# Optimization experiments

Measured on AMD Instinct MI355X. Metric: run time of the kernel, lower is better.

## Reference

```python
import jax, jax.numpy as jnp
import numpy as np

HIDDEN = 4096
NUM_HEADS = 32
NUM_KV_HEADS = 8
HEAD_DIM = 128
ROTARY_DIM = HEAD_DIM // 2  # partial_rotary_factor = 0.5
ROPE_THETA = 10000.0
EPS = 1e-5
T = 2048
Q_SIZE = NUM_HEADS * HEAD_DIM      # 4096
KV_SIZE = NUM_KV_HEADS * HEAD_DIM  # 1024


def setup_inputs() -> dict:
    key = jax.random.key(0)
    ks = jax.random.split(key, 6)
    s_in = 1.0 / np.sqrt(HIDDEN)
    s_o = 1.0 / np.sqrt(Q_SIZE)
    return {
        "positions": jnp.arange(T, dtype=jnp.int64),
        "hidden_states": jax.random.normal(ks[0], (T, HIDDEN), dtype=jnp.float32),
        "w_qkv": jax.random.normal(ks[1], (Q_SIZE + 2 * KV_SIZE, HIDDEN), dtype=jnp.float32) * s_in,
        "b_qkv": jax.random.normal(ks[2], (Q_SIZE + 2 * KV_SIZE,), dtype=jnp.float32) * 0.02,
        "q_norm_w": jnp.ones((HEAD_DIM,), dtype=jnp.float32),
        "k_norm_w": jnp.ones((HEAD_DIM,), dtype=jnp.float32),
        "w_o": jax.random.normal(ks[3], (HIDDEN, Q_SIZE), dtype=jnp.float32) * s_o,
    }


def _rms_norm(x, w, eps=EPS):
    # x: [..., head_dim]
    var = jnp.mean(x * x, axis=-1, keepdims=True)
    return x * jax.lax.rsqrt(var + eps) * w


def _apply_rope(x, positions):
    # x: [T, H, head_dim]; NeoX-style rotation on first ROTARY_DIM dims
    half = ROTARY_DIM // 2
    inv_freq = 1.0 / (ROPE_THETA ** (jnp.arange(0, ROTARY_DIM, 2, dtype=jnp.float32) / ROTARY_DIM))
    freqs = positions.astype(jnp.float32)[:, None] * inv_freq[None, :]  # [T, half]
    cos = jnp.cos(freqs)[:, None, :]  # [T, 1, half]
    sin = jnp.sin(freqs)[:, None, :]
    x_rot, x_pass = x[..., :ROTARY_DIM], x[..., ROTARY_DIM:]
    x1, x2 = x_rot[..., :half], x_rot[..., half:]
    rot = jnp.concatenate([x1 * cos - x2 * sin, x2 * cos + x1 * sin], axis=-1)
    return jnp.concatenate([rot, x_pass], axis=-1)


def reference(positions, hidden_states, w_qkv, b_qkv, q_norm_w, k_norm_w, w_o):
    qkv = hidden_states @ w_qkv.T + b_qkv  # [T, Q+2KV]
    q = qkv[:, :Q_SIZE].reshape(T, NUM_HEADS, HEAD_DIM)
    k = qkv[:, Q_SIZE:Q_SIZE + KV_SIZE].reshape(T, NUM_KV_HEADS, HEAD_DIM)
    v = qkv[:, Q_SIZE + KV_SIZE:].reshape(T, NUM_KV_HEADS, HEAD_DIM)

    q = _rms_norm(q, q_norm_w)
    k = _rms_norm(k, k_norm_w)

    q = _apply_rope(q, positions)
    k = _apply_rope(k, positions)

    # GQA: expand kv heads to match q heads
    rep = NUM_HEADS // NUM_KV_HEADS
    k = jnp.repeat(k, rep, axis=1)  # [T, H, D]
    v = jnp.repeat(v, rep, axis=1)

    scale = HEAD_DIM ** -0.5
    scores = jnp.einsum('qhd,khd->hqk', q, k) * scale  # [H, T, T]
    causal = positions[:, None] >= positions[None, :]  # [T, T]
    scores = jnp.where(causal[None, :, :], scores, jnp.float32(-1e30))
    probs = jax.nn.softmax(scores, axis=-1)
    attn = jnp.einsum('hqk,khd->qhd', probs, v).reshape(T, Q_SIZE)
    return attn @ w_o.T
```

## Files before the change

kernel.cpp:

```cpp
#include <hip/hip_runtime.h>
#include <stdint.h>

#define T_SEQ 2048
#define HIDDEN 4096
#define NUM_HEADS 32
#define NUM_KV 8
#define HD 128
#define QSIZE (NUM_HEADS * HD)
#define KVSIZE (NUM_KV * HD)
#define QKV_N (QSIZE + 2 * KVSIZE)

typedef __attribute__((ext_vector_type(8))) __bf16 bf16x8;
typedef __attribute__((ext_vector_type(4))) float f32x4;

static __device__ __forceinline__ unsigned short f2bf(float f) {
  union { float f; unsigned int u; } v; v.f = f;
  unsigned int u = v.u;
  return (unsigned short)((u + 0x7FFFu + ((u >> 16) & 1u)) >> 16);
}

static __device__ __forceinline__ void async16(const void* g, void* l) {
  __builtin_amdgcn_global_load_lds((__attribute__((address_space(1))) void*)g,
                                   (__attribute__((address_space(3))) void*)l,
                                   16, 0, 0);
}

static __device__ __forceinline__ bf16x8 lds_frag(const unsigned short* p) {
  return *(const bf16x8*)p;
}

#define N1 (T_SEQ * HIDDEN / 4)
#define N2 (QKV_N * HIDDEN / 4)
#define N3 (HIDDEN * QSIZE / 4)
__global__ void cvt_all(const float* __restrict__ h,
                        const float* __restrict__ wq,
                        const float* __restrict__ wo,
                        unsigned short* __restrict__ hb,
                        unsigned short* __restrict__ wqb,
                        unsigned short* __restrict__ wob) {
  int i = blockIdx.x * 256 + threadIdx.x;
  const float* src;
  unsigned short* dst;
  int j;
  if (i < N1) { src = h; dst = hb; j = i; }
  else if (i < N1 + N2) { src = wq; dst = wqb; j = i - N1; }
  else { src = wo; dst = wob; j = i - N1 - N2; }
  float4 f = ((const float4*)src)[j];
  ushort4 o;
  o.x = f2bf(f.x); o.y = f2bf(f.y); o.z = f2bf(f.z); o.w = f2bf(f.w);
  ((ushort4*)dst)[j] = o;
}

__global__ __launch_bounds__(256) void gemm_bt(
    const unsigned short* __restrict__ A,
    const unsigned short* __restrict__ Bt,
    const float* __restrict__ bias,
    float* __restrict__ C, int M, int N, int K) {
  __shared__ unsigned short lds_a[128 * 32];
  __shared__ unsigned short lds_b[128 * 32];
  const int tid = threadIdx.x;
  const int wave = tid >> 6, lane = tid & 63;
  const int quad = lane >> 4, l16 = lane & 15;
  const int row0 = blockIdx.x * 128, col0 = blockIdx.y * 128;
  const int wm = (wave >> 1) * 64, wn = (wave & 1) * 64;

  f32x4 acc[4][4] = {};

  const int e0 = wave * 1024 + lane * 8;
  const int e1 = e0 + 512;
  const unsigned short* Ab0 = A + (size_t)(row0 + (e0 >> 5)) * K + (e0 & 31);
  const unsigned short* Ab1 = A + (size_t)(row0 + (e1 >> 5)) * K + (e1 & 31);
  const unsigned short* Bb0 = Bt + (size_t)(col0 + (e0 >> 5)) * K + (e0 & 31);
  const unsigned short* Bb1 = Bt + (size_t)(col0 + (e1 >> 5)) * K + (e1 & 31);
  unsigned short* la0 = lds_a + wave * 1024;
  unsigned short* la1 = la0 + 512;
  unsigned short* lb0 = lds_b + wave * 1024;
  unsigned short* lb1 = lb0 + 512;

  for (int k0 = 0; k0 < K; k0 += 32) {
    __syncthreads();
    async16(Ab0 + k0, la0);
    async16(Ab1 + k0, la1);
    async16(Bb0 + k0, lb0);
    async16(Bb1 + k0, lb1);
    __syncthreads();
    bf16x8 af[4], bfr[4];
#pragma unroll
    for (int mt = 0; mt < 4; mt++)
      af[mt] = lds_frag(lds_a + (wm + mt * 16 + l16) * 32 + quad * 8);
#pragma unroll
    for (int nt = 0; nt < 4; nt++)
      bfr[nt] = lds_frag(lds_b + (wn + nt * 16 + l16) * 32 + quad * 8);
#pragma unroll
    for (int mt = 0; mt < 4; mt++)
#pragma unroll
      for (int nt = 0; nt < 4; nt++)
        acc[mt][nt] = __builtin_amdgcn_mfma_f32_16x16x32_bf16(
            af[mt], bfr[nt], acc[mt][nt], 0, 0, 0);
  }

#pragma unroll
  for (int mt = 0; mt < 4; mt++) {
#pragma unroll
    for (int nt = 0; nt < 4; nt++) {
      const int c = col0 + wn + nt * 16 + l16;
      const float bv = bias ? bias[c] : 0.0f;
      const int rbase = row0 + wm + mt * 16 + quad * 4;
#pragma unroll
      for (int r = 0; r < 4; r++)
        C[(size_t)(rbase + r) * N + c] = acc[mt][nt][r] + bv;
    }
  }
}

__global__ __launch_bounds__(256) void gemm_bt_splitk(
    const unsigned short* __restrict__ A,
    const unsigned short* __restrict__ Bt,
    float* __restrict__ C, int M, int N, int K, int kslice) {
  __shared__ unsigned short lds_a[128 * 32];
  __shared__ unsigned short lds_b[128 * 32];
  const int tid = threadIdx.x;
  const int wave = tid >> 6, lane = tid & 63;
  const int quad = lane >> 4, l16 = lane & 15;
  const int row0 = blockIdx.x * 128, col0 = blockIdx.y * 128;
  const int kofs = blockIdx.z * kslice;
  const int wm = (wave >> 1) * 64, wn = (wave & 1) * 64;

  f32x4 acc[4][4] = {};

  const int e0 = wave * 1024 + lane * 8;
  const int e1 = e0 + 512;
  const unsigned short* Ab0 = A + (size_t)(row0 + (e0 >> 5)) * K + kofs + (e0 & 31);
  const unsigned short* Ab1 = A + (size_t)(row0 + (e1 >> 5)) * K + kofs + (e1 & 31);
  const unsigned short* Bb0 = Bt + (size_t)(col0 + (e0 >> 5)) * K + kofs + (e0 & 31);
  const unsigned short* Bb1 = Bt + (size_t)(col0 + (e1 >> 5)) * K + kofs + (e1 & 31);
  unsigned short* la0 = lds_a + wave * 1024;
  unsigned short* la1 = la0 + 512;
  unsigned short* lb0 = lds_b + wave * 1024;
  unsigned short* lb1 = lb0 + 512;

  for (int k0 = 0; k0 < kslice; k0 += 32) {
    __syncthreads();
    async16(Ab0 + k0, la0);
    async16(Ab1 + k0, la1);
    async16(Bb0 + k0, lb0);
    async16(Bb1 + k0, lb1);
    __syncthreads();
    bf16x8 af[4], bfr[4];
#pragma unroll
    for (int mt = 0; mt < 4; mt++)
      af[mt] = lds_frag(lds_a + (wm + mt * 16 + l16) * 32 + quad * 8);
#pragma unroll
    for (int nt = 0; nt < 4; nt++)
      bfr[nt] = lds_frag(lds_b + (wn + nt * 16 + l16) * 32 + quad * 8);
#pragma unroll
    for (int mt = 0; mt < 4; mt++)
#pragma unroll
      for (int nt = 0; nt < 4; nt++)
        acc[mt][nt] = __builtin_amdgcn_mfma_f32_16x16x32_bf16(
            af[mt], bfr[nt], acc[mt][nt], 0, 0, 0);
  }

#pragma unroll
  for (int mt = 0; mt < 4; mt++) {
#pragma unroll
    for (int nt = 0; nt < 4; nt++) {
      const int c = col0 + wn + nt * 16 + l16;
      const int rbase = row0 + wm + mt * 16 + quad * 4;
#pragma unroll
      for (int r = 0; r < 4; r++)
        unsafeAtomicAdd(&C[(size_t)(rbase + r) * N + c], acc[mt][nt][r]);
    }
  }
}

__global__ void norm_rope(const float* __restrict__ qkv,
                          const float* __restrict__ qw,
                          const float* __restrict__ kw,
                          unsigned short* __restrict__ q,
                          unsigned short* __restrict__ k) {
  const int slot = blockIdx.x;
  const int t = blockIdx.y;
  const int d = threadIdx.x;
  const float* src = (slot < 32)
      ? qkv + (size_t)t * QKV_N + slot * HD
      : qkv + (size_t)t * QKV_N + QSIZE + (slot - 32) * HD;
  float x = src[d];
  __shared__ float red[2];
  __shared__ float ylds[HD];
  float ss = x * x;
#pragma unroll
  for (int m = 32; m >= 1; m >>= 1) ss += __shfl_xor(ss, m, 64);
  if ((d & 63) == 0) red[d >> 6] = ss;
  __syncthreads();
  const float rn = rsqrtf((red[0] + red[1]) * (1.0f / 128.0f) + 1e-5f);
  const float* w = (slot < 32) ? qw : kw;
  const float y = x * rn * w[d];
  ylds[d] = y;
  __syncthreads();
  float out;
  if (d < 64) {
    const int j = d & 31;
    const float inv = exp2f(-(float)j * (13.28771237954945f / 32.0f));
    const float ang = (float)t * inv;
    float s, c;
    sincosf(ang, &s, &c);
    const float x1 = ylds[j], x2 = ylds[j + 32];
    out = (d < 32) ? (x1 * c - x2 * s) : (x2 * c + x1 * s);
  } else {
    out = y;
  }
  if (slot < 32) q[((size_t)slot * T_SEQ + t) * HD + d] = f2bf(out);
  else           k[((size_t)(slot - 32) * T_SEQ + t) * HD + d] = f2bf(out);
}

__global__ __launch_bounds__(256) void transpose_v(
    const float* __restrict__ qkv, unsigned short* __restrict__ vt) {
  __shared__ unsigned short tile[64 * 136];
  const int kvh = blockIdx.x, tt = blockIdx.y;
  const int tid = threadIdx.x;
  {
    const int t_r = tid >> 2, d0 = (tid & 3) * 32;
    const float* src = qkv + (size_t)(tt * 64 + t_r) * QKV_N +
                       (QSIZE + KVSIZE) + kvh * HD + d0;
#pragma unroll
    for (int i = 0; i < 8; i++) {
      float4 f = ((const float4*)src)[i];
      unsigned short* dptr = tile + t_r * 136 + d0 + i * 4;
      dptr[0] = f2bf(f.x); dptr[1] = f2bf(f.y);
      dptr[2] = f2bf(f.z); dptr[3] = f2bf(f.w);
    }
  }
  __syncthreads();
  {
    const int d_r = tid >> 1, t0 = (tid & 1) * 32;
    unsigned short buf[32];
#pragma unroll
    for (int i = 0; i < 32; i++) buf[i] = tile[(t0 + i) * 136 + d_r];
    uint4* dst = (uint4*)(vt + ((size_t)kvh * HD + d_r) * T_SEQ + tt * 64 + t0);
#pragma unroll
    for (int i = 0; i < 4; i++) dst[i] = ((uint4*)buf)[i];
  }
}

#define BC 64
#define KCH 528
#define VCH 544
#define PST 72
__global__ __launch_bounds__(256) void attn_fwd(
    const unsigned short* __restrict__ Q,
    const unsigned short* __restrict__ K,
    const unsigned short* __restrict__ Vt,
    unsigned short* __restrict__ O) {
  __shared__ unsigned short lds_k[16 * KCH];
  __shared__ unsigned short lds_v[16 * VCH];
  __shared__ unsigned short lds_p[4 * 32 * PST];

  const int bx = blockIdx.x;
  const int qb = 15 - (bx >> 5);
  const int h = bx & 31;
  const int kvh = h >> 2;
  const int tid = threadIdx.x, wave = tid >> 6, lane = tid & 63;
  const int quad = lane >> 4, l16 = lane & 15;
  const int q0 = qb * 128;
  const int mrow0 = q0 + wave * 32;

  bf16x8 qf[2][4];
#pragma unroll
  for (int m = 0; m < 2; m++) {
    const unsigned short* qp =
        Q + ((size_t)h * T_SEQ + mrow0 + m * 16 + l16) * HD + quad * 8;
#pragma unroll
    for (int c2 = 0; c2 < 4; c2++) qf[m][c2] = *(const bf16x8*)(qp + c2 * 32);
  }

  f32x4 o_acc[2][8] = {};
  float lrow[2][4] = {};
  const float l2e_s = 1.4426950408889634f * 0.08838834764831845f;
  const float FMAX = 129.0f;
  const unsigned short* kb = K + (size_t)kvh * T_SEQ * HD;
  const unsigned short* vtb = Vt + (size_t)kvh * HD * T_SEQ;
  unsigned short* pbase = lds_p + wave * 32 * PST;

  const int nkt = 2 * (qb + 1);
  for (int kt = 0; kt < nkt; kt++) {
    const int kbase = kt * BC;
    __syncthreads();
#pragma unroll
    for (int cc = 0; cc < 4; cc++) {
      const int c = wave + cc * 4;
      async16(kb + (size_t)(kbase + c * 4 + (lane >> 4)) * HD + (lane & 15) * 8,
              lds_k + c * KCH + lane * 8);
      async16(vtb + (size_t)(c * 8 + (lane >> 3)) * T_SEQ + kbase + (lane & 7) * 8,
              lds_v + c * VCH + lane * 8);
    }
    __syncthreads();

    if (kbase > mrow0 + 31) continue;

    f32x4 s[2][4] = {};
#pragma unroll
    for (int c2 = 0; c2 < 4; c2++) {
#pragma unroll
      for (int nt = 0; nt < 4; nt++) {
        bf16x8 kf = lds_frag(lds_k + (nt * 4 + (l16 >> 2)) * KCH +
                             (l16 & 3) * 128 + c2 * 32 + quad * 8);
        s[0][nt] = __builtin_amdgcn_mfma_f32_16x16x32_bf16(qf[0][c2], kf, s[0][nt], 0, 0, 0);
        s[1][nt] = __builtin_amdgcn_mfma_f32_16x16x32_bf16(qf[1][c2], kf, s[1][nt], 0, 0, 0);
      }
    }

    const bool domask = (kbase + 63 > mrow0);
#pragma unroll
    for (int m = 0; m < 2; m++) {
#pragma unroll
      for (int r = 0; r < 4; r++) {
        const int row = mrow0 + m * 16 + quad * 4 + r;
        float ps = 0.f;
        unsigned short* pw = pbase + (m * 16 + quad * 4 + r) * PST + l16;
#pragma unroll
        for (int nt = 0; nt < 4; nt++) {
          float x = s[m][nt][r];
          if (domask && (kbase + nt * 16 + l16 > row)) x = -INFINITY;
          const float p = exp2f((x - FMAX) * l2e_s);
          ps += p;
          pw[nt * 16] = f2bf(p);
        }
        lrow[m][r] += ps;
      }
    }

#pragma unroll
    for (int ks = 0; ks < 2; ks++) {
      bf16x8 pa0 = lds_frag(pbase + l16 * PST + ks * 32 + quad * 8);
      bf16x8 pa1 = lds_frag(pbase + (16 + l16) * PST + ks * 32 + quad * 8);
#pragma unroll
      for (int dt = 0; dt < 8; dt++) {
        bf16x8 vf = lds_frag(lds_v + (dt * 2 + (l16 >> 3)) * VCH +
                             (l16 & 7) * 64 + ks * 32 + quad * 8);
        o_acc[0][dt] = __builtin_amdgcn_mfma_f32_16x16x32_bf16(pa0, vf, o_acc[0][dt], 0, 0, 0);
        o_acc[1][dt] = __builtin_amdgcn_mfma_f32_16x16x32_bf16(pa1, vf, o_acc[1][dt], 0, 0, 0);
      }
    }
  }

#pragma unroll
  for (int m = 0; m < 2; m++) {
#pragma unroll
    for (int r = 0; r < 4; r++) {
      float l = lrow[m][r];
#pragma unroll
      for (int msk = 1; msk < 16; msk <<= 1) l += __shfl_xor(l, msk, 16);
      const float inv = 1.0f / l;
      const int row = mrow0 + m * 16 + quad * 4 + r;
#pragma unroll
      for (int dt = 0; dt < 8; dt++)
        O[(size_t)row * QSIZE + h * HD + dt * 16 + l16] =
            f2bf(o_acc[m][dt][r] * inv);
    }
  }
}

extern "C" void kernel_launch(void* const* d_in, const int* in_sizes, int n_in,
                              void* d_out, int out_size, void* d_ws, size_t ws_size,
                              hipStream_t stream) {
  const float* hidden = (const float*)d_in[1];
  const float* w_qkv  = (const float*)d_in[2];
  const float* b_qkv  = (const float*)d_in[3];
  const float* q_norm = (const float*)d_in[4];
  const float* k_norm = (const float*)d_in[5];
  const float* w_o    = (const float*)d_in[6];
  float* out = (float*)d_out;

  char* ws = (char*)d_ws;
  unsigned short* hidden_bf = (unsigned short*)(ws + 0);
  unsigned short* wqkv_bf   = (unsigned short*)(ws + 16777216);
  unsigned short* wo_bf     = (unsigned short*)(ws + 67108864);
  float*          qkv_f32   = (float*)(ws + 100663296);
  unsigned short* q_bf      = (unsigned short*)(ws + 150994944);
  unsigned short* k_bf      = (unsigned short*)(ws + 167772160);
  unsigned short* vt_bf     = (unsigned short*)(ws + 171966464);
  unsigned short* attn_bf   = (unsigned short*)(ws + 176160768);

  hipMemsetAsync(out, 0, (size_t)T_SEQ * HIDDEN * sizeof(float), stream);

  cvt_all<<<(N1 + N2 + N3 + 255) / 256, 256, 0, stream>>>(
      hidden, w_qkv, w_o, hidden_bf, wqkv_bf, wo_bf);

  gemm_bt<<<dim3(T_SEQ / 128, QKV_N / 128), 256, 0, stream>>>(
      hidden_bf, wqkv_bf, b_qkv, qkv_f32, T_SEQ, QKV_N, HIDDEN);

  norm_rope<<<dim3(40, T_SEQ), 128, 0, stream>>>(
      qkv_f32, q_norm, k_norm, q_bf, k_bf);

  transpose_v<<<dim3(8, T_SEQ / 64), 256, 0, stream>>>(qkv_f32, vt_bf);

  attn_fwd<<<dim3(512), 256, 0, stream>>>(q_bf, k_bf, vt_bf, attn_bf);

  gemm_bt_splitk<<<dim3(T_SEQ / 128, HIDDEN / 128, 2), 256, 0, stream>>>(
      attn_bf, wo_bf, out, T_SEQ, HIDDEN, QSIZE, QSIZE / 2);
}
```

Measured before the change: 639.7 us.

## Replace split-K atomics with partial buffer plus reduce, rewrite norm_rope per-token

The output projection split-K GEMM now writes each K-half into its own buffer (the output and a reused qkv workspace region) with plain stores. A separate vectorized reduce kernel then adds them, which removes the memset and the atomic adds. norm_rope is restructured so one 256-thread block handles all 40 heads of a token, with each wave processing whole heads using shuffles instead of LDS and syncthreads. The cost is an extra kernel launch and an extra read-modify-write pass over a 32MB buffer.

```diff
diff --git a/kernel.cpp b/kernel.cpp
--- a/kernel.cpp
+++ b/kernel.cpp
@@ -116,7 +116,8 @@
 __global__ __launch_bounds__(256) void gemm_bt_splitk(
     const unsigned short* __restrict__ A,
     const unsigned short* __restrict__ Bt,
-    float* __restrict__ C, int M, int N, int K, int kslice) {
+    float* __restrict__ C0, float* __restrict__ C1,
+    int M, int N, int K, int kslice) {
   __shared__ unsigned short lds_a[128 * 32];
   __shared__ unsigned short lds_b[128 * 32];
   const int tid = threadIdx.x;
@@ -124,6 +125,7 @@
   const int quad = lane >> 4, l16 = lane & 15;
   const int row0 = blockIdx.x * 128, col0 = blockIdx.y * 128;
   const int kofs = blockIdx.z * kslice;
+  float* __restrict__ C = blockIdx.z ? C1 : C0;
   const int wm = (wave >> 1) * 64, wn = (wave & 1) * 64;
 
   f32x4 acc[4][4] = {};
@@ -169,49 +171,55 @@
       const int rbase = row0 + wm + mt * 16 + quad * 4;
 #pragma unroll
       for (int r = 0; r < 4; r++)
-        unsafeAtomicAdd(&C[(size_t)(rbase + r) * N + c], acc[mt][nt][r]);
-    }
-  }
-}
-
-__global__ void norm_rope(const float* __restrict__ qkv,
-                          const float* __restrict__ qw,
-                          const float* __restrict__ kw,
-                          unsigned short* __restrict__ q,
-                          unsigned short* __restrict__ k) {
-  const int slot = blockIdx.x;
-  const int t = blockIdx.y;
-  const int d = threadIdx.x;
-  const float* src = (slot < 32)
-      ? qkv + (size_t)t * QKV_N + slot * HD
-      : qkv + (size_t)t * QKV_N + QSIZE + (slot - 32) * HD;
-  float x = src[d];
-  __shared__ float red[2];
-  __shared__ float ylds[HD];
-  float ss = x * x;
-#pragma unroll
-  for (int m = 32; m >= 1; m >>= 1) ss += __shfl_xor(ss, m, 64);
-  if ((d & 63) == 0) red[d >> 6] = ss;
-  __syncthreads();
-  const float rn = rsqrtf((red[0] + red[1]) * (1.0f / 128.0f) + 1e-5f);
-  const float* w = (slot < 32) ? qw : kw;
-  const float y = x * rn * w[d];
-  ylds[d] = y;
-  __syncthreads();
-  float out;
-  if (d < 64) {
-    const int j = d & 31;
+        C[(size_t)(rbase + r) * N + c] = acc[mt][nt][r];
+    }
+  }
+}
+
+__global__ void reduce_add(float* __restrict__ out,
+                           const float* __restrict__ part, int n4) {
+  int i = blockIdx.x * 256 + threadIdx.x;
+  if (i >= n4) return;
+  float4 a = ((const float4*)out)[i];
+  float4 b = ((const float4*)part)[i];
+  a.x += b.x; a.y += b.y; a.z += b.z; a.w += b.w;
+  ((float4*)out)[i] = a;
+}
+
+__global__ __launch_bounds__(256) void norm_rope(
+    const float* __restrict__ qkv,
+    const float* __restrict__ qw,
+    const float* __restrict__ kw,
+    unsigned short* __restrict__ q,
+    unsigned short* __restrict__ k) {
+  const int t = blockIdx.x;
+  const int wave = threadIdx.x >> 6, lane = threadIdx.x & 63;
+#pragma unroll
+  for (int it = 0; it < 10; it++) {
+    const int slot = it * 4 + wave;
+    const bool isq = slot < 32;
+    const float* src = qkv + (size_t)t * QKV_N +
+                       (isq ? slot * HD : QSIZE + (slot - 32) * HD);
+    const float x0 = src[lane];
+    const float x1 = src[lane + 64];
+    float ss = x0 * x0 + x1 * x1;
+#pragma unroll
+    for (int m = 32; m >= 1; m >>= 1) ss += __shfl_xor(ss, m, 64);
+    const float rn = rsqrtf(ss * (1.0f / 128.0f) + 1e-5f);
+    const float* w = isq ? qw : kw;
+    const float y0 = x0 * rn * w[lane];
+    const float y1 = x1 * rn * w[lane + 64];
+    const float p = __shfl_xor(y0, 32, 64);
+    const int j = lane & 31;
     const float inv = exp2f(-(float)j * (13.28771237954945f / 32.0f));
-    const float ang = (float)t * inv;
     float s, c;
-    sincosf(ang, &s, &c);
-    const float x1 = ylds[j], x2 = ylds[j + 32];
-    out = (d < 32) ? (x1 * c - x2 * s) : (x2 * c + x1 * s);
-  } else {
-    out = y;
-  }
-  if (slot < 32) q[((size_t)slot * T_SEQ + t) * HD + d] = f2bf(out);
-  else           k[((size_t)(slot - 32) * T_SEQ + t) * HD + d] = f2bf(out);
+    sincosf((float)t * inv, &s, &c);
+    const float r0 = (lane < 32) ? (y0 * c - p * s) : (y0 * c + p * s);
+    unsigned short* dst = isq ? q + ((size_t)slot * T_SEQ + t) * HD
+                              : k + ((size_t)(slot - 32) * T_SEQ + t) * HD;
+    dst[lane] = f2bf(r0);
+    dst[lane + 64] = f2bf(y1);
+  }
 }
 
 __global__ __launch_bounds__(256) void transpose_v(
@@ -381,8 +389,7 @@
   unsigned short* k_bf      = (unsigned short*)(ws + 167772160);
   unsigned short* vt_bf     = (unsigned short*)(ws + 171966464);
   unsigned short* attn_bf   = (unsigned short*)(ws + 176160768);
-
-  hipMemsetAsync(out, 0, (size_t)T_SEQ * HIDDEN * sizeof(float), stream);
+  float*          part_f32  = (float*)(ws + 100663296);
 
   cvt_all<<<(N1 + N2 + N3 + 255) / 256, 256, 0, stream>>>(
       hidden, w_qkv, w_o, hidden_bf, wqkv_bf, wo_bf);
@@ -390,7 +397,7 @@
   gemm_bt<<<dim3(T_SEQ / 128, QKV_N / 128), 256, 0, stream>>>(
       hidden_bf, wqkv_bf, b_qkv, qkv_f32, T_SEQ, QKV_N, HIDDEN);
 
-  norm_rope<<<dim3(40, T_SEQ), 128, 0, stream>>>(
+  norm_rope<<<dim3(T_SEQ), 256, 0, stream>>>(
       qkv_f32, q_norm, k_norm, q_bf, k_bf);
 
   transpose_v<<<dim3(8, T_SEQ / 64), 256, 0, stream>>>(qkv_f32, vt_bf);
@@ -398,5 +405,8 @@
   attn_fwd<<<dim3(512), 256, 0, stream>>>(q_bf, k_bf, vt_bf, attn_bf);
 
   gemm_bt_splitk<<<dim3(T_SEQ / 128, HIDDEN / 128, 2), 256, 0, stream>>>(
-      attn_bf, wo_bf, out, T_SEQ, HIDDEN, QSIZE, QSIZE / 2);
-}
+      attn_bf, wo_bf, out, part_f32, T_SEQ, HIDDEN, QSIZE, QSIZE / 2);
+
+  reduce_add<<<(T_SEQ * HIDDEN / 4 + 255) / 256, 256, 0, stream>>>(
+      out, part_f32, T_SEQ * HIDDEN / 4);
+}
```

After: 610.2 us. 1.05x faster.
